# Performance work log

Hardware: AMD Instinct MI355X
Metric: run time of the kernel (lower is better)

## Reference

```python
import jax, jax.numpy as jnp
import numpy as np

B, NV, NS, L = 32, 2048, 512, 64
FEAT, SEM, HID, ATT, DM = 1024, 512, 512, 512, 512


def setup_inputs() -> dict:
    key = jax.random.key(0)
    ks = jax.random.split(key, 14)
    s = lambda k, sh: jax.random.normal(k, sh, dtype=jnp.float32) * 0.02
    return {
        "query": jax.random.normal(ks[0], (B, 1, HID), dtype=jnp.float32),
        "visual_features": jax.random.normal(ks[1], (B, NV, FEAT), dtype=jnp.float32),
        "semantic_features": jax.random.normal(ks[2], (B, NS, SEM), dtype=jnp.float32),
        "patient_info": jax.random.normal(ks[3], (B, L, DM), dtype=jnp.float32),
        "W1v": s(ks[4], (HID, ATT)),
        "W2v": s(ks[5], (FEAT, ATT)),
        "vv": s(ks[6], (ATT, 1)),
        "W3": s(ks[7], (DM, ATT)),
        "b3": jnp.zeros((ATT,), dtype=jnp.float32),
        "W1s": s(ks[8], (HID, ATT)),
        "W2s": s(ks[9], (SEM, ATT)),
        "vs": s(ks[10], (ATT, 1)),
        "W": s(ks[11], (FEAT + SEM, FEAT)),
        "bW": jnp.zeros((FEAT,), dtype=jnp.float32),
    }


def reference(query, visual_features, semantic_features, patient_info,
              W1v, W2v, vv, W3, b3, W1s, W2s, vs, W, bW):
    # mean over patient sequence, project: [B,1,ATT]
    pinfo = jnp.mean(patient_info, axis=1, keepdims=True) @ W3 + b3
    q_v = query @ W1v          # [B,1,ATT]
    # visual branch
    v_scores = jnp.tanh(q_v + visual_features @ W2v + pinfo) @ vv  # [B,NV,1]
    v_attn = jax.nn.softmax(v_scores, axis=1)
    # semantic branch
    q_s = query @ W1s
    s_scores = jnp.tanh(q_s + semantic_features @ W2s + pinfo) @ vs  # [B,NS,1]
    s_attn = jax.nn.softmax(s_scores, axis=1)
    ctx = jnp.concatenate([
        jnp.sum(visual_features * v_attn, axis=1),    # [B,FEAT]
        jnp.sum(semantic_features * s_attn, axis=1),  # [B,SEM]
    ], axis=1) @ W + bW
    return ctx, v_attn, s_attn
```

## Files before the change

### kernel.cpp

```cpp
#include <hip/hip_runtime.h>

typedef float f32x4 __attribute__((ext_vector_type(4)));
typedef short short8 __attribute__((ext_vector_type(8)));

#define B_    32
#define NV_   2048
#define NS_   512
#define L_    64
#define FEAT_ 1024
#define SEM_  512
#define HID_  512
#define ATT_  512
#define DM_   512

__device__ __forceinline__ unsigned int f2bf_pk(float lo, float hi) {
  unsigned int ul = (__float_as_uint(lo) + 0x8000u) >> 16;
  unsigned int uh = (__float_as_uint(hi) + 0x8000u) & 0xffff0000u;
  return uh | ul;
}

__device__ __forceinline__ unsigned short f2bf(float f) {
  return (unsigned short)((__float_as_uint(f) + 0x8000u) >> 16);
}

__device__ __forceinline__ float bflo(unsigned int u) { return __uint_as_float(u << 16); }
__device__ __forceinline__ float bfhi(unsigned int u) { return __uint_as_float(u & 0xffff0000u); }

__device__ __forceinline__ float fast_tanh(float x) {
  float e = __expf(2.f * x);
  return 1.f - 2.f * __builtin_amdgcn_rcpf(e + 1.f);
}

__global__ __launch_bounds__(256) void k_pmean(const float* __restrict__ pat,
                                               float* __restrict__ pm) {
  int b = blockIdx.x, t = threadIdx.x;
  for (int d = t; d < DM_; d += 256) {
    float s = 0.f;
    for (int l = 0; l < L_; ++l) s += pat[(b * L_ + l) * DM_ + d];
    pm[b * DM_ + d] = s * (1.f / 64.f);
  }
}

__global__ __launch_bounds__(256) void k_qp(const float* __restrict__ query,
                                            const float* __restrict__ pm,
                                            const float* __restrict__ W1v,
                                            const float* __restrict__ W1s,
                                            const float* __restrict__ W3,
                                            const float* __restrict__ b3,
                                            float* __restrict__ qpv,
                                            float* __restrict__ qps) {
  int idx = blockIdx.x * 256 + threadIdx.x;
  int b = idx >> 9, a = idx & 511;
  float pi = b3[a];
  for (int d = 0; d < DM_; ++d) pi += pm[b * DM_ + d] * W3[d * ATT_ + a];
  float qv = 0.f, qs = 0.f;
  for (int h = 0; h < HID_; ++h) {
    float q = query[b * HID_ + h];
    qv += q * W1v[h * ATT_ + a];
    qs += q * W1s[h * ATT_ + a];
  }
  qpv[idx] = qv + pi;
  qps[idx] = qs + pi;
}

__global__ __launch_bounds__(256) void k_swz(const float* __restrict__ W2,
                                             unsigned short* __restrict__ out,
                                             int total) {
  int idx = blockIdx.x * 256 + threadIdx.x;
  if (idx >= total) return;
  int k = idx >> 9, c = idx & 511;
  int kc = k >> 5, kr = k & 31, q = kr >> 3, j = kr & 7;
  int cb = c >> 4, n = c & 15;
  out[(kc * 32 + cb) * 512 + q * 128 + n * 8 + j] = f2bf(W2[idx]);
}

__global__ __launch_bounds__(256, 2) void k_scores_fused(
    const float* __restrict__ X, const unsigned short* __restrict__ Wt,
    const float* __restrict__ qp, const float* __restrict__ vvec,
    float* __restrict__ score, unsigned short* __restrict__ Av,
    int K, int rows_per_batch) {
  __shared__ __align__(16) unsigned short As[2048];
  const int t = threadIdx.x;
  const int lane = t & 63, wave = t >> 6;
  const int quad = lane >> 4, l15 = lane & 15;
  const int row0 = blockIdx.x * 64;
  const int b = row0 / rows_per_batch;
  const int nk = K >> 5;
  const int rt128 = blockIdx.x >> 1;
  const int rbOff = (blockIdx.x & 1) * 4;

  const int r = t >> 2, q_ = t & 3;
  const int arb = r >> 4, am = r & 15;
  const float* gA = X + (size_t)(row0 + r) * K + q_ * 8;
  uint4* asDst = (uint4*)(As + arb * 512 + q_ * 128 + am * 8);
  char* avBase = (char*)(Av + (size_t)rt128 * nk * 4096) +
                 (rbOff + arb) * 1024 + q_ * 256 + am * 16;

  const char* gB = (const char*)Wt + (size_t)wave * 8192 + lane * 16;

  const f32x4 zero = {0.f, 0.f, 0.f, 0.f};
  f32x4 acc[4][8];
#pragma unroll
  for (int a = 0; a < 4; ++a)
#pragma unroll
    for (int cb = 0; cb < 8; ++cb) acc[a][cb] = zero;

  for (int kc = 0; kc < nk; ++kc) {
    short8 bfr[8];
    const char* gBk = gB + (size_t)kc * 32768;
#pragma unroll
    for (int cb = 0; cb < 8; ++cb)
      bfr[cb] = *(const short8*)(gBk + cb * 1024);

    __syncthreads();
    const float4 v0 = *(const float4*)(gA + kc * 32);
    const float4 v1 = *(const float4*)(gA + kc * 32 + 4);
    uint4 o;
    o.x = f2bf_pk(v0.x, v0.y);
    o.y = f2bf_pk(v0.z, v0.w);
    o.z = f2bf_pk(v1.x, v1.y);
    o.w = f2bf_pk(v1.z, v1.w);
    *asDst = o;
    *(uint4*)(avBase + (size_t)kc * 8192) = o;
    __syncthreads();

    short8 af[4];
#pragma unroll
    for (int a = 0; a < 4; ++a)
      af[a] = *(const short8*)(As + a * 512 + quad * 128 + l15 * 8);
#pragma unroll
    for (int a = 0; a < 4; ++a)
#pragma unroll
      for (int cb = 0; cb < 8; ++cb)
        acc[a][cb] = __builtin_amdgcn_mfma_f32_16x16x32_bf16(af[a], bfr[cb], acc[a][cb], 0, 0, 0);
  }

  float qv_[8], vw_[8];
#pragma unroll
  for (int cb = 0; cb < 8; ++cb) {
    int col = wave * 128 + cb * 16 + l15;
    qv_[cb] = qp[b * ATT_ + col];
    vw_[cb] = vvec[col];
  }
#pragma unroll
  for (int a = 0; a < 4; ++a) {
#pragma unroll
    for (int rr = 0; rr < 4; ++rr) {
      float s = 0.f;
#pragma unroll
      for (int cb = 0; cb < 8; ++cb)
        s += fast_tanh(acc[a][cb][rr] + qv_[cb]) * vw_[cb];
      s += __shfl_xor(s, 1);
      s += __shfl_xor(s, 2);
      s += __shfl_xor(s, 4);
      s += __shfl_xor(s, 8);
      if (l15 == 0) atomicAdd(&score[row0 + a * 16 + quad * 4 + rr], s);
    }
  }
}

__global__ __launch_bounds__(256) void k_scores_f32(const float* __restrict__ X,
                                                    const unsigned short* __restrict__ Wt,
                                                    const float* __restrict__ qp,
                                                    const float* __restrict__ vvec,
                                                    float* __restrict__ score,
                                                    int K, int rows_per_batch) {
  __shared__ __align__(16) unsigned short As[4096];
  __shared__ __align__(16) unsigned short Bs[4096];
  const int t = threadIdx.x;
  const int lane = t & 63;
  const int wave = t >> 6;
  const int wr = wave & 1, wc = wave >> 1;
  const int quad = lane >> 4, l15 = lane & 15;
  const int row0 = blockIdx.x * 128;
  const int ct = blockIdx.y;
  const int b = row0 / rows_per_batch;

  const int ai_row = t >> 3;
  const int ai_k0 = (t & 7) * 4;
  const int a_q = ai_k0 >> 3;
  const int a_j0 = ai_k0 & 7;

  const f32x4 zero = {0.f, 0.f, 0.f, 0.f};
  f32x4 acc[4][4];
#pragma unroll
  for (int a = 0; a < 4; ++a)
#pragma unroll
    for (int bb = 0; bb < 4; ++bb) acc[a][bb] = zero;

  const int nk = K >> 5;
  for (int kc = 0; kc < nk; ++kc) {
    __syncthreads();
#pragma unroll
    for (int ii = 0; ii < 4; ++ii) {
      int i = ii * 32 + ai_row;
      const float4 v = *(const float4*)(X + (size_t)(row0 + i) * K + kc * 32 + ai_k0);
      uint2 h;
      h.x = f2bf_pk(v.x, v.y);
      h.y = f2bf_pk(v.z, v.w);
      int rb = i >> 4, m = i & 15;
      *(uint2*)(As + rb * 512 + a_q * 128 + m * 8 + a_j0) = h;
    }
    {
      const uint4* src = (const uint4*)(Wt + (size_t)(kc * 32 + ct * 8) * 512);
      uint4* dst = (uint4*)Bs;
      dst[t] = src[t];
      dst[t + 256] = src[t + 256];
    }
    __syncthreads();
    short8 af[4], bfr[4];
#pragma unroll
    for (int a = 0; a < 4; ++a)
      af[a] = *(const short8*)(As + (wr * 4 + a) * 512 + quad * 128 + l15 * 8);
#pragma unroll
    for (int bb = 0; bb < 4; ++bb)
      bfr[bb] = *(const short8*)(Bs + (wc * 4 + bb) * 512 + quad * 128 + l15 * 8);
#pragma unroll
    for (int a = 0; a < 4; ++a)
#pragma unroll
      for (int bb = 0; bb < 4; ++bb)
        acc[a][bb] = __builtin_amdgcn_mfma_f32_16x16x32_bf16(af[a], bfr[bb], acc[a][bb], 0, 0, 0);
  }

  const int colbase = ct * 128 + wc * 64;
  float qv_[4], vw_[4];
#pragma unroll
  for (int bb = 0; bb < 4; ++bb) {
    int col = colbase + bb * 16 + l15;
    qv_[bb] = qp[b * ATT_ + col];
    vw_[bb] = vvec[col];
  }
#pragma unroll
  for (int a = 0; a < 4; ++a) {
#pragma unroll
    for (int r = 0; r < 4; ++r) {
      float s = 0.f;
#pragma unroll
      for (int bb = 0; bb < 4; ++bb)
        s += fast_tanh(acc[a][bb][r] + qv_[bb]) * vw_[bb];
      s += __shfl_xor(s, 1);
      s += __shfl_xor(s, 2);
      s += __shfl_xor(s, 4);
      s += __shfl_xor(s, 8);
      if (l15 == 0) {
        int row = row0 + wr * 64 + a * 16 + quad * 4 + r;
        atomicAdd(&score[row], s);
      }
    }
  }
}

__global__ __launch_bounds__(256) void k_softmax(const float* __restrict__ score,
                                                 float* __restrict__ attn, int N) {
  __shared__ float sm[4];
  int b = blockIdx.x, t = threadIdx.x;
  const float* s = score + (size_t)b * N;
  float m = -1e30f;
  for (int i = t; i < N; i += 256) m = fmaxf(m, s[i]);
  for (int k = 32; k; k >>= 1) m = fmaxf(m, __shfl_xor(m, k));
  if ((t & 63) == 0) sm[t >> 6] = m;
  __syncthreads();
  m = fmaxf(fmaxf(sm[0], sm[1]), fmaxf(sm[2], sm[3]));
  __syncthreads();
  float sum = 0.f;
  for (int i = t; i < N; i += 256) sum += __expf(s[i] - m);
  for (int k = 32; k; k >>= 1) sum += __shfl_xor(sum, k);
  if ((t & 63) == 0) sm[t >> 6] = sum;
  __syncthreads();
  sum = sm[0] + sm[1] + sm[2] + sm[3];
  float inv = 1.f / sum;
  for (int i = t; i < N; i += 256) attn[(size_t)b * N + i] = __expf(s[i] - m) * inv;
}

__global__ __launch_bounds__(256) void k_wsum_swz(const unsigned short* __restrict__ Aswz,
                                                  const float* __restrict__ attn,
                                                  float* __restrict__ ctx_pre,
                                                  int nkc, int rtPerBatch,
                                                  int rowsPerBatch, int colOff) {
  const int b = blockIdx.x, kc = blockIdx.y;
  const int t = threadIdx.x, q = t >> 6, l = t & 63;
  const int rbl = l >> 4, m = l & 15;
  float acc[8] = {0.f, 0.f, 0.f, 0.f, 0.f, 0.f, 0.f, 0.f};
  for (int rt = 0; rt < rtPerBatch; ++rt) {
    const unsigned short* blk = Aswz + ((size_t)(b * rtPerBatch + rt) * nkc + kc) * 4096;
    const float* ab = attn + (size_t)b * rowsPerBatch + rt * 128;
#pragma unroll
    for (int p = 0; p < 2; ++p) {
      int rb = p * 4 + rbl;
      float a = ab[rb * 16 + m];
      uint4 v = *(const uint4*)(blk + rb * 512 + q * 128 + m * 8);
      acc[0] += a * bflo(v.x);
      acc[1] += a * bfhi(v.x);
      acc[2] += a * bflo(v.y);
      acc[3] += a * bfhi(v.y);
      acc[4] += a * bflo(v.z);
      acc[5] += a * bfhi(v.z);
      acc[6] += a * bflo(v.w);
      acc[7] += a * bfhi(v.w);
    }
  }
#pragma unroll
  for (int off = 1; off < 64; off <<= 1) {
#pragma unroll
    for (int j = 0; j < 8; ++j) acc[j] += __shfl_xor(acc[j], off);
  }
  if (l == 0) {
    float* dst = ctx_pre + b * 1536 + colOff + kc * 32 + q * 8;
#pragma unroll
    for (int j = 0; j < 8; ++j) dst[j] = acc[j];
  }
}

__global__ __launch_bounds__(256) void k_wsum(const float* __restrict__ feats,
                                              const float* __restrict__ attn,
                                              float* __restrict__ ctx_pre,
                                              int N, int F, int colOff, int rowsPerChunk) {
  int b = blockIdx.x, rc = blockIdx.y, t = threadIdx.x;
  int c4 = t * 4;
  if (c4 >= F) return;
  int r0 = rc * rowsPerChunk;
  const float* fb = feats + ((size_t)b * N + r0) * F;
  const float* ab = attn + (size_t)b * N + r0;
  float4 acc = {0.f, 0.f, 0.f, 0.f};
  for (int r = 0; r < rowsPerChunk; ++r) {
    float a = ab[r];
    float4 v = *(const float4*)(fb + (size_t)r * F + c4);
    acc.x += a * v.x; acc.y += a * v.y; acc.z += a * v.z; acc.w += a * v.w;
  }
  float* dst = ctx_pre + b * 1536 + colOff + c4;
  atomicAdd(dst + 0, acc.x);
  atomicAdd(dst + 1, acc.y);
  atomicAdd(dst + 2, acc.z);
  atomicAdd(dst + 3, acc.w);
}

__global__ __launch_bounds__(256) void k_final(const float* __restrict__ cp,
                                               const float* __restrict__ W,
                                               const float* __restrict__ bW,
                                               float* __restrict__ out) {
  int b = blockIdx.x, oc = blockIdx.y, t = threadIdx.x;
  int o = oc * 256 + t;
  float acc = bW[o];
  const float* c = cp + b * 1536;
  for (int k = 0; k < 1536; ++k) acc += c[k] * W[k * FEAT_ + o];
  out[b * FEAT_ + o] = acc;
}

extern "C" void kernel_launch(void* const* d_in, const int* in_sizes, int n_in,
                              void* d_out, int out_size, void* d_ws, size_t ws_size,
                              hipStream_t stream) {
  const float* query = (const float*)d_in[0];
  const float* vf    = (const float*)d_in[1];
  const float* sf    = (const float*)d_in[2];
  const float* pat   = (const float*)d_in[3];
  const float* W1v   = (const float*)d_in[4];
  const float* W2v   = (const float*)d_in[5];
  const float* vv    = (const float*)d_in[6];
  const float* W3    = (const float*)d_in[7];
  const float* b3    = (const float*)d_in[8];
  const float* W1s   = (const float*)d_in[9];
  const float* W2s   = (const float*)d_in[10];
  const float* vs    = (const float*)d_in[11];
  const float* W     = (const float*)d_in[12];
  const float* bW    = (const float*)d_in[13];
  float* out = (float*)d_out;

  char* ws = (char*)d_ws;
  float* scores_v = (float*)(ws);
  float* scores_s = (float*)(ws + 262144);
  float* ctx_pre  = (float*)(ws + 327680);
  float* pm   = (float*)(ws + 524288);
  float* qpv  = (float*)(ws + 589824);
  float* qps  = (float*)(ws + 655360);
  unsigned short* Wtv = (unsigned short*)(ws + 720896);
  unsigned short* Wts = (unsigned short*)(ws + 720896 + 1048576);
  unsigned short* Av  = (unsigned short*)(ws + 4194304);
  unsigned short* Asm = (unsigned short*)(ws + 4194304 + 134217728);
  const size_t NEED = 4194304ull + 134217728ull + 16777216ull;
  const bool bf16path = (ws_size >= NEED);

  hipMemsetAsync(d_ws, 0, bf16path ? 327680 : 524288, stream);

  k_pmean<<<32, 256, 0, stream>>>(pat, pm);
  k_qp<<<64, 256, 0, stream>>>(query, pm, W1v, W1s, W3, b3, qpv, qps);
  k_swz<<<(FEAT_ * ATT_) / 256, 256, 0, stream>>>(W2v, Wtv, FEAT_ * ATT_);
  k_swz<<<(SEM_ * ATT_) / 256, 256, 0, stream>>>(W2s, Wts, SEM_ * ATT_);

  float* v_attn = out + B_ * FEAT_;
  float* s_attn = out + B_ * FEAT_ + B_ * NV_;

  if (bf16path) {
    k_scores_fused<<<(B_ * NV_) / 64, 256, 0, stream>>>(vf, Wtv, qpv, vv, scores_v, Av, FEAT_, NV_);
    k_scores_fused<<<(B_ * NS_) / 64, 256, 0, stream>>>(sf, Wts, qps, vs, scores_s, Asm, SEM_, NS_);
    k_softmax<<<B_, 256, 0, stream>>>(scores_v, v_attn, NV_);
    k_softmax<<<B_, 256, 0, stream>>>(scores_s, s_attn, NS_);
    k_wsum_swz<<<dim3(B_, FEAT_ / 32), 256, 0, stream>>>(Av, v_attn, ctx_pre, FEAT_ / 32, NV_ / 128, NV_, 0);
    k_wsum_swz<<<dim3(B_, SEM_ / 32), 256, 0, stream>>>(Asm, s_attn, ctx_pre, SEM_ / 32, NS_ / 128, NS_, 1024);
  } else {
    k_scores_f32<<<dim3((B_ * NV_) / 128, 4), 256, 0, stream>>>(vf, Wtv, qpv, vv, scores_v, FEAT_, NV_);
    k_scores_f32<<<dim3((B_ * NS_) / 128, 4), 256, 0, stream>>>(sf, Wts, qps, vs, scores_s, SEM_, NS_);
    k_softmax<<<B_, 256, 0, stream>>>(scores_v, v_attn, NV_);
    k_softmax<<<B_, 256, 0, stream>>>(scores_s, s_attn, NS_);
    k_wsum<<<dim3(B_, 8), 256, 0, stream>>>(vf, v_attn, ctx_pre, NV_, FEAT_, 0, 256);
    k_wsum<<<dim3(B_, 2), 256, 0, stream>>>(sf, s_attn, ctx_pre, NS_, SEM_, 1024, 256);
  }

  k_final<<<dim3(B_, 4), 256, 0, stream>>>(ctx_pre, W, bW, out);
}
```

Before: 685.7 us.

## Double-buffer A tile in LDS with register prefetch and XOR swizzle

The scores kernel now prefetches X rows two k-steps ahead into registers, double-buffers the bf16 A tile in shared memory so one barrier per iteration suffices, and XOR-swizzles the LDS layout to reduce bank conflicts. It also drops the min-blocks-per-CU launch bound. The aim is to hide global load latency behind the MFMA loop and cut synchronisation. In exchange it raises register pressure and may lower occupancy, and it relies on a hand-written waitcnt/barrier sequence.

```diff
diff --git a/kernel.cpp b/kernel.cpp
--- a/kernel.cpp
+++ b/kernel.cpp
@@ -74,12 +74,12 @@
   out[(kc * 32 + cb) * 512 + q * 128 + n * 8 + j] = f2bf(W2[idx]);
 }
 
-__global__ __launch_bounds__(256, 2) void k_scores_fused(
+__global__ __launch_bounds__(256) void k_scores_fused(
     const float* __restrict__ X, const unsigned short* __restrict__ Wt,
     const float* __restrict__ qp, const float* __restrict__ vvec,
     float* __restrict__ score, unsigned short* __restrict__ Av,
     int K, int rows_per_batch) {
-  __shared__ __align__(16) unsigned short As[2048];
+  __shared__ __align__(16) unsigned short As[2][2048];
   const int t = threadIdx.x;
   const int lane = t & 63, wave = t >> 6;
   const int quad = lane >> 4, l15 = lane & 15;
@@ -91,19 +91,24 @@
 
   const int r = t >> 2, q_ = t & 3;
   const int arb = r >> 4, am = r & 15;
-  const float* gA = X + (size_t)(row0 + r) * K + q_ * 8;
-  uint4* asDst = (uint4*)(As + arb * 512 + q_ * 128 + am * 8);
+  const float4* gA4 = (const float4*)(X + (size_t)(row0 + r) * K + q_ * 8);
+  const int aoff = arb * 512 + q_ * 128 + ((am ^ (q_ << 1)) * 8);
   char* avBase = (char*)(Av + (size_t)rt128 * nk * 4096) +
                  (rbOff + arb) * 1024 + q_ * 256 + am * 16;
 
   const char* gB = (const char*)Wt + (size_t)wave * 8192 + lane * 16;
 
+  const int afoff = quad * 128 + ((l15 ^ (quad << 1)) * 8);
+
   const f32x4 zero = {0.f, 0.f, 0.f, 0.f};
   f32x4 acc[4][8];
 #pragma unroll
   for (int a = 0; a < 4; ++a)
 #pragma unroll
     for (int cb = 0; cb < 8; ++cb) acc[a][cb] = zero;
+
+  float4 c0 = gA4[0], c1 = gA4[1];
+  float4 p0 = gA4[8], p1 = gA4[9];
 
   for (int kc = 0; kc < nk; ++kc) {
     short8 bfr[8];
@@ -112,27 +117,34 @@
     for (int cb = 0; cb < 8; ++cb)
       bfr[cb] = *(const short8*)(gBk + cb * 1024);
 
-    __syncthreads();
-    const float4 v0 = *(const float4*)(gA + kc * 32);
-    const float4 v1 = *(const float4*)(gA + kc * 32 + 4);
+    const int kn = (kc + 2 < nk) ? kc + 2 : nk - 1;
+    const float4 n0 = gA4[kn * 8];
+    const float4 n1 = gA4[kn * 8 + 1];
+
     uint4 o;
-    o.x = f2bf_pk(v0.x, v0.y);
-    o.y = f2bf_pk(v0.z, v0.w);
-    o.z = f2bf_pk(v1.x, v1.y);
-    o.w = f2bf_pk(v1.z, v1.w);
-    *asDst = o;
+    o.x = f2bf_pk(c0.x, c0.y);
+    o.y = f2bf_pk(c0.z, c0.w);
+    o.z = f2bf_pk(c1.x, c1.y);
+    o.w = f2bf_pk(c1.z, c1.w);
+    *(uint4*)(&As[kc & 1][aoff]) = o;
     *(uint4*)(avBase + (size_t)kc * 8192) = o;
-    __syncthreads();
+
+    asm volatile("s_waitcnt lgkmcnt(0)" ::: "memory");
+    __builtin_amdgcn_s_barrier();
+    asm volatile("" ::: "memory");
 
     short8 af[4];
 #pragma unroll
     for (int a = 0; a < 4; ++a)
-      af[a] = *(const short8*)(As + a * 512 + quad * 128 + l15 * 8);
+      af[a] = *(const short8*)(&As[kc & 1][a * 512 + afoff]);
 #pragma unroll
     for (int a = 0; a < 4; ++a)
 #pragma unroll
       for (int cb = 0; cb < 8; ++cb)
         acc[a][cb] = __builtin_amdgcn_mfma_f32_16x16x32_bf16(af[a], bfr[cb], acc[a][cb], 0, 0, 0);
+
+    c0 = p0; c1 = p1;
+    p0 = n0; p1 = n1;
   }
 
   float qv_[8], vw_[8];
```

Measured after the change: 711.3 us. 3.7% more time.

## Triple-buffer activation tiles via async global-to-LDS loads in fused scores kernel

Applied to the files above, without the earlier changes.

The fused scores kernel now streams fp32 activation tiles straight into a three-stage LDS ring with global_load_lds, prefetching two k-steps ahead. Each wave converts to bf16 when it reads its MFMA fragments from a swizzled layout, and only wave 0 writes the bf16 copy used later. This drops one of the two block barriers per k-step and hides global load latency behind the MFMAs. In exchange it triples the LDS footprint, keeps the tiles in fp32, and relies on implicit vmcnt waits to order the async copies.

```diff
diff --git a/kernel.cpp b/kernel.cpp
--- a/kernel.cpp
+++ b/kernel.cpp
@@ -13,6 +13,8 @@
 #define ATT_  512
 #define DM_   512
 
+#define FENCE asm volatile("" ::: "memory")
+
 __device__ __forceinline__ unsigned int f2bf_pk(float lo, float hi) {
   unsigned int ul = (__float_as_uint(lo) + 0x8000u) >> 16;
   unsigned int uh = (__float_as_uint(hi) + 0x8000u) & 0xffff0000u;
@@ -29,6 +31,12 @@
 __device__ __forceinline__ float fast_tanh(float x) {
   float e = __expf(2.f * x);
   return 1.f - 2.f * __builtin_amdgcn_rcpf(e + 1.f);
+}
+
+__device__ __forceinline__ void gload16(const void* g, void* l) {
+  __builtin_amdgcn_global_load_lds(
+      (const __attribute__((address_space(1))) unsigned char*)g,
+      (__attribute__((address_space(3))) unsigned char*)l, 16, 0, 0);
 }
 
 __global__ __launch_bounds__(256) void k_pmean(const float* __restrict__ pat,
@@ -79,7 +87,7 @@
     const float* __restrict__ qp, const float* __restrict__ vvec,
     float* __restrict__ score, unsigned short* __restrict__ Av,
     int K, int rows_per_batch) {
-  __shared__ __align__(16) unsigned short As[2048];
+  __shared__ __align__(16) float AsF[3 * 2048];
   const int t = threadIdx.x;
   const int lane = t & 63, wave = t >> 6;
   const int quad = lane >> 4, l15 = lane & 15;
@@ -89,13 +97,17 @@
   const int rt128 = blockIdx.x >> 1;
   const int rbOff = (blockIdx.x & 1) * 4;
 
-  const int r = t >> 2, q_ = t & 3;
-  const int arb = r >> 4, am = r & 15;
-  const float* gA = X + (size_t)(row0 + r) * K + q_ * 8;
-  uint4* asDst = (uint4*)(As + arb * 512 + q_ * 128 + am * 8);
-  char* avBase = (char*)(Av + (size_t)rt128 * nk * 4096) +
-                 (rbOff + arb) * 1024 + q_ * 256 + am * 16;
-
+  const int g_hi = lane >> 3, g_lo = lane & 7;
+  const int sub = g_lo ^ (g_hi & 7);
+  const int kofs = (sub >> 1) * 8 + (sub & 1) * 4;
+  const float* gsrc0 = X + (size_t)(row0 + wave * 16 + g_hi) * K + kofs;
+  const float* gsrc1 = X + (size_t)(row0 + wave * 16 + 8 + g_hi) * K + kofs;
+
+  const int swz = (l15 & 7) << 4;
+  const int ro0 = (l15 * 128 + quad * 32) ^ swz;
+  const int ro1 = (l15 * 128 + quad * 32 + 16) ^ swz;
+
+  char* avB = (char*)(Av + (size_t)rt128 * nk * 4096) + rbOff * 1024 + quad * 256 + l15 * 16;
   const char* gB = (const char*)Wt + (size_t)wave * 8192 + lane * 16;
 
   const f32x4 zero = {0.f, 0.f, 0.f, 0.f};
@@ -104,6 +116,16 @@
   for (int a = 0; a < 4; ++a)
 #pragma unroll
     for (int cb = 0; cb < 8; ++cb) acc[a][cb] = zero;
+
+  {
+    char* d0 = (char*)AsF + wave * 2048;
+    gload16(gsrc0, d0);
+    gload16(gsrc1, d0 + 1024);
+    char* d1 = (char*)AsF + 8192 + wave * 2048;
+    gload16(gsrc0 + 32, d1);
+    gload16(gsrc1 + 32, d1 + 1024);
+  }
+  asm volatile("s_waitcnt vmcnt(2)" ::: "memory");
 
   for (int kc = 0; kc < nk; ++kc) {
     short8 bfr[8];
@@ -112,27 +134,41 @@
     for (int cb = 0; cb < 8; ++cb)
       bfr[cb] = *(const short8*)(gBk + cb * 1024);
 
-    __syncthreads();
-    const float4 v0 = *(const float4*)(gA + kc * 32);
-    const float4 v1 = *(const float4*)(gA + kc * 32 + 4);
-    uint4 o;
-    o.x = f2bf_pk(v0.x, v0.y);
-    o.y = f2bf_pk(v0.z, v0.w);
-    o.z = f2bf_pk(v1.x, v1.y);
-    o.w = f2bf_pk(v1.z, v1.w);
-    *asDst = o;
-    *(uint4*)(avBase + (size_t)kc * 8192) = o;
-    __syncthreads();
-
-    short8 af[4];
-#pragma unroll
-    for (int a = 0; a < 4; ++a)
-      af[a] = *(const short8*)(As + a * 512 + quad * 128 + l15 * 8);
-#pragma unroll
-    for (int a = 0; a < 4; ++a)
+    FENCE;
+    __builtin_amdgcn_s_barrier();
+    FENCE;
+
+    const char* bufR = (const char*)AsF + (kc % 3) * 8192;
+    uint4 u[4];
+#pragma unroll
+    for (int a = 0; a < 4; ++a) {
+      f32x4 lo = *(const f32x4*)(bufR + a * 2048 + ro0);
+      f32x4 hi = *(const f32x4*)(bufR + a * 2048 + ro1);
+      uint4 v;
+      v.x = f2bf_pk(lo.x, lo.y);
+      v.y = f2bf_pk(lo.z, lo.w);
+      v.z = f2bf_pk(hi.x, hi.y);
+      v.w = f2bf_pk(hi.z, hi.w);
+      u[a] = v;
+    }
+    if (wave == 0) {
+      char* avK = avB + (size_t)kc * 8192;
+#pragma unroll
+      for (int a = 0; a < 4; ++a) *(uint4*)(avK + a * 1024) = u[a];
+    }
+#pragma unroll
+    for (int a = 0; a < 4; ++a) {
+      short8 af = (short8&)u[a];
 #pragma unroll
       for (int cb = 0; cb < 8; ++cb)
-        acc[a][cb] = __builtin_amdgcn_mfma_f32_16x16x32_bf16(af[a], bfr[cb], acc[a][cb], 0, 0, 0);
+        acc[a][cb] = __builtin_amdgcn_mfma_f32_16x16x32_bf16(af, bfr[cb], acc[a][cb], 0, 0, 0);
+    }
+
+    if (kc + 2 < nk) {
+      char* d = (char*)AsF + ((kc + 2) % 3) * 8192 + wave * 2048;
+      gload16(gsrc0 + (size_t)(kc + 2) * 32, d);
+      gload16(gsrc1 + (size_t)(kc + 2) * 32, d + 1024);
+    }
   }
 
   float qv_[8], vw_[8];
```

New measurement: 686.5 us. Within noise of the previous version (+0.1%).
